# Kernel tuning notes

Measured on AMD Instinct MI355X. Metric: run time of the kernel, lower is better.

The kernel has to match this reference:

```python
import jax, jax.numpy as jnp
import numpy as np

B, N, D, E, R, K = 4, 2048, 1024, 8, 256, 2


def setup_inputs() -> dict:
    key = jax.random.key(0)
    ks = jax.random.split(key, 5)
    scale = 0.02
    return {
        "x": jax.random.normal(ks[0], (B, N, D), dtype=jnp.float32),
        "gate_w": jax.random.normal(ks[1], (D, E), dtype=jnp.float32) * scale,
        "Wu": jax.random.normal(ks[2], (E, D, R), dtype=jnp.float32) * scale,
        "Wv": jax.random.normal(ks[3], (E, D, R), dtype=jnp.float32) * scale,
        "Wo": jax.random.normal(ks[4], (E, R, D), dtype=jnp.float32) * scale,
    }


def reference(x, gate_w, Wu, Wv, Wo):
    # Router: top-k over expert logits, softmax over the selected k logits.
    logits = jnp.einsum("bnd,de->bne", x, gate_w)          # [B,N,E]
    topv, topi = jax.lax.top_k(logits, K)                    # [B,N,K]
    w = jax.nn.softmax(topv, axis=-1)                        # [B,N,K]

    # Dense all-expert SwiGLU (matches reference semantics: every expert
    # computed for every token, then gathered by top-k index).
    u = jnp.einsum("bnd,edr->bner", x, Wu)                  # [B,N,E,R]
    v = jnp.einsum("bnd,edr->bner", x, Wv)                  # [B,N,E,R]
    s = jax.nn.silu(u) * v                                   # [B,N,E,R]
    Y = jnp.einsum("bner,erd->bned", s, Wo)                 # [B,N,E,D]

    # Gather the k selected experts per token and combine with gate weights.
    y_sel = jnp.take_along_axis(Y, topi[..., None], axis=2)  # [B,N,K,D]
    out = jnp.einsum("bnkd,bnk->bnd", y_sel, w)             # [B,N,D]
    return out
```

## Files before the change

### kernel.cpp

```cpp
#include <hip/hip_runtime.h>
#include <math.h>

#define BN 8192
#define DIM 1024
#define NE 8
#define RR 256

using bf16x8 = __attribute__((ext_vector_type(8))) short;
using f32x4  = __attribute__((ext_vector_type(4))) float;

#define GLD16(g, l) __builtin_amdgcn_global_load_lds(                      \
    (const __attribute__((address_space(1))) void*)(g),                    \
    (__attribute__((address_space(3))) void*)(l), 16, 0, 0)

__device__ inline unsigned short f2bf(float f) {
    unsigned int u = __float_as_uint(f);
    u = (u + 0x7fffu + ((u >> 16) & 1u)) >> 16;
    return (unsigned short)u;
}

__global__ __launch_bounds__(256) void k_gwt(const float* __restrict__ gw,
                                             float* __restrict__ gwT) {
    int i = blockIdx.x * 256 + threadIdx.x;
    float v = gw[i];
    int d = i >> 3, e = i & 7;
    gwT[e * DIM + d] = v;
}

__global__ __launch_bounds__(256) void k_router3(const float* __restrict__ x,
                                                 const float* __restrict__ gwT,
                                                 int* __restrict__ topi,
                                                 float* __restrict__ topw,
                                                 unsigned short* __restrict__ xb) {
    int wid  = (blockIdx.x * blockDim.x + threadIdx.x) >> 6;
    int lane = threadIdx.x & 63;
    const float* xp = x + (size_t)wid * DIM + lane * 4;
    unsigned short* xbp = xb + (size_t)wid * DIM + lane * 4;
    float4 acc[NE];
#pragma unroll
    for (int e = 0; e < NE; ++e) acc[e] = float4{0.f, 0.f, 0.f, 0.f};
#pragma unroll
    for (int k = 0; k < 4; ++k) {
        float4 xv = *(const float4*)(xp + k * 256);
        ushort4 us = { f2bf(xv.x), f2bf(xv.y), f2bf(xv.z), f2bf(xv.w) };
        *(ushort4*)(xbp + k * 256) = us;
#pragma unroll
        for (int e = 0; e < NE; ++e) {
            float4 gv = *(const float4*)(gwT + e * DIM + k * 256 + lane * 4);
            acc[e].x += xv.x * gv.x; acc[e].y += xv.y * gv.y;
            acc[e].z += xv.z * gv.z; acc[e].w += xv.w * gv.w;
        }
    }
    float lg[NE];
#pragma unroll
    for (int e = 0; e < NE; ++e)
        lg[e] = (acc[e].x + acc[e].y) + (acc[e].z + acc[e].w);
#pragma unroll
    for (int off = 32; off; off >>= 1) {
#pragma unroll
        for (int e = 0; e < NE; ++e) lg[e] += __shfl_xor(lg[e], off, 64);
    }
    if (lane == 0) {
        float best = lg[0]; int bi = 0;
#pragma unroll
        for (int e = 1; e < NE; ++e) if (lg[e] > best) { best = lg[e]; bi = e; }
        float sec = -3.4e38f; int si = 0;
#pragma unroll
        for (int e = 0; e < NE; ++e) if (e != bi && lg[e] > sec) { sec = lg[e]; si = e; }
        float p  = __expf(sec - best);
        float w0 = 1.f / (1.f + p);
        float w1 = p * w0;
        topi[wid * 2 + 0] = bi;  topw[wid * 2 + 0] = w0;
        topi[wid * 2 + 1] = si;  topw[wid * 2 + 1] = w1;
    }
}

__global__ __launch_bounds__(1024) void k_count_scan(const int* __restrict__ topi,
                                                     int* __restrict__ counts,
                                                     int* __restrict__ offsets,
                                                     int* __restrict__ fill,
                                                     int* __restrict__ tileOff) {
    __shared__ int sh[1024 * NE];
    int tid = threadIdx.x;
    int c[NE];
#pragma unroll
    for (int j = 0; j < NE; ++j) c[j] = 0;
    const int4* tp = (const int4*)topi;
    for (int i = tid; i < BN * 2 / 4; i += 1024) {
        int4 v = tp[i];
#pragma unroll
        for (int j = 0; j < NE; ++j)
            c[j] += (v.x == j) + (v.y == j) + (v.z == j) + (v.w == j);
    }
#pragma unroll
    for (int j = 0; j < NE; ++j) sh[tid * NE + j] = c[j];
    __syncthreads();
    for (int s = 512; s > 0; s >>= 1) {
        if (tid < s) {
#pragma unroll
            for (int j = 0; j < NE; ++j) sh[tid * NE + j] += sh[(tid + s) * NE + j];
        }
        __syncthreads();
    }
    if (tid == 0) {
        int acc = 0, tacc = 0;
        for (int j = 0; j < NE; ++j) {
            int cj = sh[j];
            counts[j]  = cj;
            offsets[j] = acc;   acc  += cj;
            tileOff[j] = tacc;  tacc += (cj + 127) >> 7;
        }
        tileOff[NE] = tacc;
    }
    if (tid < NE) fill[tid] = 0;
}

__global__ __launch_bounds__(256) void k_fill2(const int* __restrict__ topi,
                                               const float* __restrict__ topw,
                                               const int* __restrict__ offsets,
                                               int* __restrict__ fill,
                                               int* __restrict__ btok,
                                               float* __restrict__ bw,
                                               int* __restrict__ slotOf) {
    int tid = threadIdx.x;
    int i = blockIdx.x * 256 + tid;
    int w = tid >> 6, lane = tid & 63;
    int e = topi[i];
    float wt = topw[i];

    __shared__ int waveCnt[4][NE];
    __shared__ int wavePre[4][NE];
    __shared__ int baseSh[NE];

    int myrank = 0;
    unsigned long long lt = (1ull << lane) - 1ull;
#pragma unroll
    for (int j = 0; j < NE; ++j) {
        unsigned long long m = __ballot(e == j);
        if (e == j) myrank = __popcll(m & lt);
        if (lane == 0) waveCnt[w][j] = __popcll(m);
    }
    __syncthreads();
    if (tid < NE) {
        int j = tid, acc = 0;
#pragma unroll
        for (int ww = 0; ww < 4; ++ww) { wavePre[ww][j] = acc; acc += waveCnt[ww][j]; }
        baseSh[j] = atomicAdd(&fill[j], acc);
    }
    __syncthreads();
    int slot = offsets[e] + baseSh[e] + wavePre[w][e] + myrank;
    btok[slot] = i >> 1;
    bw[slot]   = wt;
    slotOf[i]  = slot;
}

__global__ __launch_bounds__(256) void k_cvt3(const float* __restrict__ Wu,
                                              const float* __restrict__ Wv,
                                              const float* __restrict__ Wo,
                                              unsigned short* __restrict__ Wub,
                                              unsigned short* __restrict__ Wvb,
                                              unsigned short* __restrict__ Wob) {
    int z = blockIdx.y;
    int which = z >> 3, e = z & 7;
    int tile = blockIdx.x;
    const float* in; unsigned short* out;
    int M, N, n0, m0;
    if (which < 2) {
        M = DIM; N = RR;
        n0 = (tile & 7) * 32;  m0 = (tile >> 3) * 32;
        in = which ? Wv : Wu;  out = which ? Wvb : Wub;
    } else {
        M = RR; N = DIM;
        n0 = (tile & 31) * 32; m0 = (tile >> 5) * 32;
        in = Wo; out = Wob;
    }
    __shared__ float t[32][33];
    int tx = threadIdx.x & 31, ty = threadIdx.x >> 5;
    const float* inE = in + (size_t)e * M * N;
    unsigned short* outE = out + (size_t)e * M * N;
#pragma unroll
    for (int i = ty; i < 32; i += 8)
        t[i][tx] = inE[(size_t)(m0 + i) * N + n0 + tx];
    __syncthreads();
#pragma unroll
    for (int i = ty; i < 32; i += 8)
        outE[(size_t)(n0 + i) * M + m0 + tx] = f2bf(t[tx][i]);
}

__global__ __launch_bounds__(256, 2) void k_uv(
        const unsigned short* __restrict__ xb,
        const unsigned short* __restrict__ Wub,
        const unsigned short* __restrict__ Wvb,
        const int* __restrict__ counts,
        const int* __restrict__ offsets,
        const int* __restrict__ tileOff,
        const int* __restrict__ btok,
        const float* __restrict__ bw,
        unsigned short* __restrict__ Sbuf) {
    int bid = blockIdx.x;
    int lt  = (bid & 7) * 68 + (bid >> 3);
    int rt  = lt & 3;
    int mt_lin = lt >> 2;
    if (mt_lin >= tileOff[NE]) return;
    int e = 0;
#pragma unroll
    for (int j = 1; j < NE; ++j) if (mt_lin >= tileOff[j]) e = j;
    int t0 = (mt_lin - tileOff[e]) * 128;
    int ne = counts[e];
    int nt = min(128, ne - t0);
    int start = offsets[e] + t0;

    int tid = threadIdx.x;
    int w = tid >> 6, lane = tid & 63;
    int m16 = lane & 15, quad = lane >> 4;
    int wm = w & 1, wn = w >> 1;

    __shared__ unsigned short As[128][64];
    __shared__ unsigned short Bs[128][64];
    __shared__ int   tokL[128];
    __shared__ float gwL[128];

    if (tid < 128) {
        tokL[tid] = (tid < nt) ? btok[start + tid] : btok[start];
        gwL[tid]  = (tid < nt) ? bw[start + tid] : 0.f;
    }
    __syncthreads();

    int rc0 = rt * 64;
    const unsigned short* WuE = Wub + (size_t)e * RR * DIM;
    const unsigned short* WvE = Wvb + (size_t)e * RR * DIM;

    const unsigned short* aS[4];
    const unsigned short* bS[4];
    int dstOff[4];
#pragma unroll
    for (int i = 0; i < 4; ++i) {
        int chunk = w * 4 + i;
        int row = chunk * 8 + (lane >> 3);
        int js  = (lane & 7) ^ (row & 7);
        aS[i] = xb + (size_t)tokL[row] * DIM + js * 8;
        bS[i] = ((row < 64) ? (WuE + (size_t)(rc0 + row) * DIM)
                            : (WvE + (size_t)(rc0 + row - 64) * DIM)) + js * 8;
        dstOff[i] = chunk * 1024;
    }
    auto* asb = (__attribute__((address_space(3))) char*)&As[0][0];
    auto* bsb = (__attribute__((address_space(3))) char*)&Bs[0][0];
    const char* Ab = (const char*)&As[0][0];
    const char* Bb = (const char*)&Bs[0][0];

    f32x4 accU[4][2], accV[4][2];
    f32x4 zz = {0.f, 0.f, 0.f, 0.f};
#pragma unroll
    for (int mt = 0; mt < 4; ++mt)
#pragma unroll
        for (int nl = 0; nl < 2; ++nl) { accU[mt][nl] = zz; accV[mt][nl] = zz; }

    for (int kt = 0; kt < 16; ++kt) {
        if (kt) __syncthreads();
#pragma unroll
        for (int i = 0; i < 4; ++i) {
            GLD16(aS[i] + kt * 64, asb + dstOff[i]);
            GLD16(bS[i] + kt * 64, bsb + dstOff[i]);
        }
        __syncthreads();
#pragma unroll
        for (int ks = 0; ks < 2; ++ks) {
            bf16x8 a[4], bu[2], bv[2];
#pragma unroll
            for (int mt = 0; mt < 4; ++mt) {
                int r = wm * 64 + mt * 16 + m16;
                int u = (ks * 4 + quad) ^ (r & 7);
                a[mt] = *(const bf16x8*)(Ab + r * 128 + u * 16);
            }
#pragma unroll
            for (int nl = 0; nl < 2; ++nl) {
                int r = wn * 32 + nl * 16 + m16;
                int u = (ks * 4 + quad) ^ (r & 7);
                bu[nl] = *(const bf16x8*)(Bb + r * 128 + u * 16);
                bv[nl] = *(const bf16x8*)(Bb + (r + 64) * 128 + u * 16);
            }
#pragma unroll
            for (int nl = 0; nl < 2; ++nl)
#pragma unroll
                for (int mt = 0; mt < 4; ++mt) {
                    accU[mt][nl] = __builtin_amdgcn_mfma_f32_16x16x32_bf16(a[mt], bu[nl], accU[mt][nl], 0, 0, 0);
                    accV[mt][nl] = __builtin_amdgcn_mfma_f32_16x16x32_bf16(a[mt], bv[nl], accV[mt][nl], 0, 0, 0);
                }
        }
    }

#pragma unroll
    for (int mt = 0; mt < 4; ++mt)
#pragma unroll
        for (int nl = 0; nl < 2; ++nl)
#pragma unroll
            for (int reg = 0; reg < 4; ++reg) {
                int trow = wm * 64 + mt * 16 + quad * 4 + reg;
                int rcol = rc0 + wn * 32 + nl * 16 + m16;
                float u = accU[mt][nl][reg], v = accV[mt][nl][reg];
                float s = (u / (1.f + __expf(-u))) * v * gwL[trow];
                if (trow < nt)
                    Sbuf[(size_t)(start + trow) * RR + rcol] = f2bf(s);
            }
}

__global__ __launch_bounds__(256, 2) void k_down(
        const unsigned short* __restrict__ Sbuf,
        const unsigned short* __restrict__ Wob,
        const int* __restrict__ counts,
        const int* __restrict__ offsets,
        const int* __restrict__ tileOff,
        const int* __restrict__ btok,
        float* __restrict__ ybuf,
        float* __restrict__ out) {
    int bid = blockIdx.x;
    int lt  = (bid & 7) * 136 + (bid >> 3);
    int nd = lt & 7;
    int mt_lin = lt >> 3;
    if (mt_lin >= tileOff[NE]) return;
    int e = 0;
#pragma unroll
    for (int j = 1; j < NE; ++j) if (mt_lin >= tileOff[j]) e = j;
    int t0 = (mt_lin - tileOff[e]) * 128;
    int ne = counts[e];
    int nt = min(128, ne - t0);
    int start = offsets[e] + t0;

    int tid = threadIdx.x;
    int w = tid >> 6, lane = tid & 63;
    int m16 = lane & 15, quad = lane >> 4;
    int wm = w & 1, wn = w >> 1;

    __shared__ unsigned short As[128][64];
    __shared__ unsigned short Bs[128][64];
    __shared__ int tokL[128];

    if (tid < 128)
        tokL[tid] = (tid < nt) ? btok[start + tid] : btok[start];
    __syncthreads();

    const unsigned short* WoE = Wob + (size_t)e * DIM * RR;

    const unsigned short* aS[4];
    const unsigned short* bS[4];
    int dstOff[4];
#pragma unroll
    for (int i = 0; i < 4; ++i) {
        int chunk = w * 4 + i;
        int row = chunk * 8 + (lane >> 3);
        int js  = (lane & 7) ^ (row & 7);
        aS[i] = Sbuf + (size_t)(start + row) * RR + js * 8;
        bS[i] = WoE + (size_t)(nd * 128 + row) * RR + js * 8;
        dstOff[i] = chunk * 1024;
    }
    auto* asb = (__attribute__((address_space(3))) char*)&As[0][0];
    auto* bsb = (__attribute__((address_space(3))) char*)&Bs[0][0];
    const char* Ab = (const char*)&As[0][0];
    const char* Bb = (const char*)&Bs[0][0];

    f32x4 acc[4][4];
    f32x4 zz = {0.f, 0.f, 0.f, 0.f};
#pragma unroll
    for (int mt = 0; mt < 4; ++mt)
#pragma unroll
        for (int nl = 0; nl < 4; ++nl) acc[mt][nl] = zz;

    for (int kt = 0; kt < 4; ++kt) {
        if (kt) __syncthreads();
#pragma unroll
        for (int i = 0; i < 4; ++i) {
            GLD16(aS[i] + kt * 64, asb + dstOff[i]);
            GLD16(bS[i] + kt * 64, bsb + dstOff[i]);
        }
        __syncthreads();
#pragma unroll
        for (int ks = 0; ks < 2; ++ks) {
            bf16x8 a[4], b[4];
#pragma unroll
            for (int mt = 0; mt < 4; ++mt) {
                int r = wm * 64 + mt * 16 + m16;
                int u = (ks * 4 + quad) ^ (r & 7);
                a[mt] = *(const bf16x8*)(Ab + r * 128 + u * 16);
            }
#pragma unroll
            for (int nl = 0; nl < 4; ++nl) {
                int r = wn * 64 + nl * 16 + m16;
                int u = (ks * 4 + quad) ^ (r & 7);
                b[nl] = *(const bf16x8*)(Bb + r * 128 + u * 16);
            }
#pragma unroll
            for (int nl = 0; nl < 4; ++nl)
#pragma unroll
                for (int mt = 0; mt < 4; ++mt)
                    acc[mt][nl] = __builtin_amdgcn_mfma_f32_16x16x32_bf16(a[mt], b[nl], acc[mt][nl], 0, 0, 0);
        }
    }

    if (ybuf) {
#pragma unroll
        for (int mt = 0; mt < 4; ++mt)
#pragma unroll
            for (int nl = 0; nl < 4; ++nl)
#pragma unroll
                for (int reg = 0; reg < 4; ++reg) {
                    int srow = wm * 64 + mt * 16 + quad * 4 + reg;
                    int d    = nd * 128 + wn * 64 + nl * 16 + m16;
                    if (srow < nt)
                        ybuf[(size_t)(start + srow) * DIM + d] = acc[mt][nl][reg];
                }
    } else {
#pragma unroll
        for (int mt = 0; mt < 4; ++mt)
#pragma unroll
            for (int nl = 0; nl < 4; ++nl)
#pragma unroll
                for (int reg = 0; reg < 4; ++reg) {
                    int srow = wm * 64 + mt * 16 + quad * 4 + reg;
                    int d    = nd * 128 + wn * 64 + nl * 16 + m16;
                    if (srow < nt)
                        atomicAdd(&out[(size_t)tokL[srow] * DIM + d], acc[mt][nl][reg]);
                }
    }
}

__global__ __launch_bounds__(256) void k_combine(const float* __restrict__ ybuf,
                                                 const int* __restrict__ slotOf,
                                                 float* __restrict__ out) {
    int t   = blockIdx.x;
    int seg = threadIdx.x;
    int s0 = slotOf[t * 2 + 0];
    int s1 = slotOf[t * 2 + 1];
    float4 a = *(const float4*)(ybuf + (size_t)s0 * DIM + seg * 4);
    float4 b = *(const float4*)(ybuf + (size_t)s1 * DIM + seg * 4);
    float4 r = { a.x + b.x, a.y + b.y, a.z + b.z, a.w + b.w };
    *(float4*)(out + (size_t)t * DIM + seg * 4) = r;
}

extern "C" void kernel_launch(void* const* d_in, const int* in_sizes, int n_in,
                              void* d_out, int out_size, void* d_ws, size_t ws_size,
                              hipStream_t stream) {
    const float* x  = (const float*)d_in[0];
    const float* gw = (const float*)d_in[1];
    const float* Wu = (const float*)d_in[2];
    const float* Wv = (const float*)d_in[3];
    const float* Wo = (const float*)d_in[4];
    float* out = (float*)d_out;

    int*   wsi     = (int*)d_ws;
    int*   counts  = wsi + 0;
    int*   offsets = wsi + 8;
    int*   fill    = wsi + 16;
    int*   tileOff = wsi + 24;
    int*   topi    = wsi + 48;
    float* topw    = (float*)(wsi + 48 + 16384);
    int*   btok    = wsi + 48 + 32768;
    float* bw      = (float*)(wsi + 48 + 49152);
    int*   slotOf  = wsi + 48 + 65536;
    float* gwT     = (float*)((char*)d_ws + 327872);

    const size_t off_xb  = 393216;
    const size_t off_wub = off_xb  + (size_t)BN * DIM * 2;
    const size_t off_wvb = off_wub + (size_t)NE * RR * DIM * 2;
    const size_t off_wob = off_wvb + (size_t)NE * RR * DIM * 2;
    const size_t off_sb  = off_wob + (size_t)NE * DIM * RR * 2;
    const size_t off_yb  = off_sb  + (size_t)(BN * 2 + 128) * RR * 2;
    const size_t need_yb = off_yb  + (size_t)BN * 2 * DIM * 4;

    unsigned short* xb   = (unsigned short*)((char*)d_ws + off_xb);
    unsigned short* Wub  = (unsigned short*)((char*)d_ws + off_wub);
    unsigned short* Wvb  = (unsigned short*)((char*)d_ws + off_wvb);
    unsigned short* Wob  = (unsigned short*)((char*)d_ws + off_wob);
    unsigned short* Sbuf = (unsigned short*)((char*)d_ws + off_sb);
    bool use_ybuf = (ws_size >= need_yb);
    float* ybuf = use_ybuf ? (float*)((char*)d_ws + off_yb) : nullptr;

    k_gwt<<<dim3(DIM * NE / 256), 256, 0, stream>>>(gw, gwT);
    k_router3<<<dim3(BN / 4), 256, 0, stream>>>(x, gwT, topi, topw, xb);
    k_count_scan<<<1, 1024, 0, stream>>>(topi, counts, offsets, fill, tileOff);
    k_fill2<<<dim3(BN * 2 / 256), 256, 0, stream>>>(topi, topw, offsets, fill,
                                                    btok, bw, slotOf);
    k_cvt3<<<dim3(256, 24), 256, 0, stream>>>(Wu, Wv, Wo, Wub, Wvb, Wob);

    if (!use_ybuf)
        hipMemsetAsync(d_out, 0, (size_t)BN * DIM * sizeof(float), stream);

    k_uv<<<dim3(544), 256, 0, stream>>>(xb, Wub, Wvb, counts, offsets, tileOff,
                                        btok, bw, Sbuf);
    k_down<<<dim3(1088), 256, 0, stream>>>(Sbuf, Wob, counts, offsets, tileOff,
                                           btok, ybuf, out);
    if (use_ybuf)
        k_combine<<<dim3(BN), 256, 0, stream>>>(ybuf, slotOf, out);
}
```

Before: 195.7 us.

## Double-buffer LDS tiles in up and down projection GEMM kernels

Both grouped expert GEMM kernels now keep two LDS buffers for the A and B tiles. Each iteration issues the async global-to-LDS loads for the next k-tile before running MFMAs on the current one, with one barrier per iteration instead of two. The goal is to hide global load latency behind compute. It doubles LDS use per block (64KB), which may reduce occupancy. It also relies on the barrier waiting for the async LDS loads to finish.

```diff
diff --git a/kernel.cpp b/kernel.cpp
--- a/kernel.cpp
+++ b/kernel.cpp
@@ -215,8 +215,8 @@
     int m16 = lane & 15, quad = lane >> 4;
     int wm = w & 1, wn = w >> 1;
 
-    __shared__ unsigned short As[128][64];
-    __shared__ unsigned short Bs[128][64];
+    __shared__ unsigned short As[2][128][64];
+    __shared__ unsigned short Bs[2][128][64];
     __shared__ int   tokL[128];
     __shared__ float gwL[128];
 
@@ -243,10 +243,18 @@
                             : (WvE + (size_t)(rc0 + row - 64) * DIM)) + js * 8;
         dstOff[i] = chunk * 1024;
     }
-    auto* asb = (__attribute__((address_space(3))) char*)&As[0][0];
-    auto* bsb = (__attribute__((address_space(3))) char*)&Bs[0][0];
-    const char* Ab = (const char*)&As[0][0];
-    const char* Bb = (const char*)&Bs[0][0];
+    auto* asb = (__attribute__((address_space(3))) char*)&As[0][0][0];
+    auto* bsb = (__attribute__((address_space(3))) char*)&Bs[0][0][0];
+    const char* Ab = (const char*)&As[0][0][0];
+    const char* Bb = (const char*)&Bs[0][0][0];
+
+    auto stage = [&](int buf, int kt) {
+#pragma unroll
+        for (int i = 0; i < 4; ++i) {
+            GLD16(aS[i] + kt * 64, asb + buf * 16384 + dstOff[i]);
+            GLD16(bS[i] + kt * 64, bsb + buf * 16384 + dstOff[i]);
+        }
+    };
 
     f32x4 accU[4][2], accV[4][2];
     f32x4 zz = {0.f, 0.f, 0.f, 0.f};
@@ -255,14 +263,11 @@
 #pragma unroll
         for (int nl = 0; nl < 2; ++nl) { accU[mt][nl] = zz; accV[mt][nl] = zz; }
 
+    stage(0, 0);
+    __syncthreads();
     for (int kt = 0; kt < 16; ++kt) {
-        if (kt) __syncthreads();
-#pragma unroll
-        for (int i = 0; i < 4; ++i) {
-            GLD16(aS[i] + kt * 64, asb + dstOff[i]);
-            GLD16(bS[i] + kt * 64, bsb + dstOff[i]);
-        }
-        __syncthreads();
+        const int cur = kt & 1;
+        if (kt < 15) stage(cur ^ 1, kt + 1);
 #pragma unroll
         for (int ks = 0; ks < 2; ++ks) {
             bf16x8 a[4], bu[2], bv[2];
@@ -270,14 +275,14 @@
             for (int mt = 0; mt < 4; ++mt) {
                 int r = wm * 64 + mt * 16 + m16;
                 int u = (ks * 4 + quad) ^ (r & 7);
-                a[mt] = *(const bf16x8*)(Ab + r * 128 + u * 16);
+                a[mt] = *(const bf16x8*)(Ab + cur * 16384 + r * 128 + u * 16);
             }
 #pragma unroll
             for (int nl = 0; nl < 2; ++nl) {
                 int r = wn * 32 + nl * 16 + m16;
                 int u = (ks * 4 + quad) ^ (r & 7);
-                bu[nl] = *(const bf16x8*)(Bb + r * 128 + u * 16);
-                bv[nl] = *(const bf16x8*)(Bb + (r + 64) * 128 + u * 16);
+                bu[nl] = *(const bf16x8*)(Bb + cur * 16384 + r * 128 + u * 16);
+                bv[nl] = *(const bf16x8*)(Bb + cur * 16384 + (r + 64) * 128 + u * 16);
             }
 #pragma unroll
             for (int nl = 0; nl < 2; ++nl)
@@ -287,6 +292,7 @@
                     accV[mt][nl] = __builtin_amdgcn_mfma_f32_16x16x32_bf16(a[mt], bv[nl], accV[mt][nl], 0, 0, 0);
                 }
         }
+        __syncthreads();
     }
 
 #pragma unroll
@@ -331,8 +337,8 @@
     int m16 = lane & 15, quad = lane >> 4;
     int wm = w & 1, wn = w >> 1;
 
-    __shared__ unsigned short As[128][64];
-    __shared__ unsigned short Bs[128][64];
+    __shared__ unsigned short As[2][128][64];
+    __shared__ unsigned short Bs[2][128][64];
     __shared__ int tokL[128];
 
     if (tid < 128)
@@ -353,10 +359,18 @@
         bS[i] = WoE + (size_t)(nd * 128 + row) * RR + js * 8;
         dstOff[i] = chunk * 1024;
     }
-    auto* asb = (__attribute__((address_space(3))) char*)&As[0][0];
-    auto* bsb = (__attribute__((address_space(3))) char*)&Bs[0][0];
-    const char* Ab = (const char*)&As[0][0];
-    const char* Bb = (const char*)&Bs[0][0];
+    auto* asb = (__attribute__((address_space(3))) char*)&As[0][0][0];
+    auto* bsb = (__attribute__((address_space(3))) char*)&Bs[0][0][0];
+    const char* Ab = (const char*)&As[0][0][0];
+    const char* Bb = (const char*)&Bs[0][0][0];
+
+    auto stage = [&](int buf, int kt) {
+#pragma unroll
+        for (int i = 0; i < 4; ++i) {
+            GLD16(aS[i] + kt * 64, asb + buf * 16384 + dstOff[i]);
+            GLD16(bS[i] + kt * 64, bsb + buf * 16384 + dstOff[i]);
+        }
+    };
 
     f32x4 acc[4][4];
     f32x4 zz = {0.f, 0.f, 0.f, 0.f};
@@ -365,14 +379,11 @@
 #pragma unroll
         for (int nl = 0; nl < 4; ++nl) acc[mt][nl] = zz;
 
+    stage(0, 0);
+    __syncthreads();
     for (int kt = 0; kt < 4; ++kt) {
-        if (kt) __syncthreads();
-#pragma unroll
-        for (int i = 0; i < 4; ++i) {
-            GLD16(aS[i] + kt * 64, asb + dstOff[i]);
-            GLD16(bS[i] + kt * 64, bsb + dstOff[i]);
-        }
-        __syncthreads();
+        const int cur = kt & 1;
+        if (kt < 3) stage(cur ^ 1, kt + 1);
 #pragma unroll
         for (int ks = 0; ks < 2; ++ks) {
             bf16x8 a[4], b[4];
@@ -380,13 +391,13 @@
             for (int mt = 0; mt < 4; ++mt) {
                 int r = wm * 64 + mt * 16 + m16;
                 int u = (ks * 4 + quad) ^ (r & 7);
-                a[mt] = *(const bf16x8*)(Ab + r * 128 + u * 16);
+                a[mt] = *(const bf16x8*)(Ab + cur * 16384 + r * 128 + u * 16);
             }
 #pragma unroll
             for (int nl = 0; nl < 4; ++nl) {
                 int r = wn * 64 + nl * 16 + m16;
                 int u = (ks * 4 + quad) ^ (r & 7);
-                b[nl] = *(const bf16x8*)(Bb + r * 128 + u * 16);
+                b[nl] = *(const bf16x8*)(Bb + cur * 16384 + r * 128 + u * 16);
             }
 #pragma unroll
             for (int nl = 0; nl < 4; ++nl)
@@ -394,6 +405,7 @@
                 for (int mt = 0; mt < 4; ++mt)
                     acc[mt][nl] = __builtin_amdgcn_mfma_f32_16x16x32_bf16(a[mt], b[nl], acc[mt][nl], 0, 0, 0);
         }
+        __syncthreads();
     }
 
     if (ybuf) {
```

After: 209.2 us. +6.9%, slower.

## Fuse expert counting into router and drop gate-weight transpose kernel

Applied to the files above, without the earlier changes.

The router now reads gate_w in its native [D,E] layout, so the separate transpose kernel goes away. Per-expert counts are accumulated inside the router with shared-memory atomics followed by one global atomic per block. This replaces the single-block 1024-thread count/scan kernel with a tiny scan kernel and a memset that zeros counts and fill. The aim is fewer launches and less serial single-block work, at the cost of global atomics and a different gate-weight access pattern.

```diff
diff --git a/kernel.cpp b/kernel.cpp
--- a/kernel.cpp
+++ b/kernel.cpp
@@ -19,47 +19,44 @@
     return (unsigned short)u;
 }
 
-__global__ __launch_bounds__(256) void k_gwt(const float* __restrict__ gw,
-                                             float* __restrict__ gwT) {
-    int i = blockIdx.x * 256 + threadIdx.x;
-    float v = gw[i];
-    int d = i >> 3, e = i & 7;
-    gwT[e * DIM + d] = v;
-}
-
 __global__ __launch_bounds__(256) void k_router3(const float* __restrict__ x,
-                                                 const float* __restrict__ gwT,
+                                                 const float* __restrict__ gw,
                                                  int* __restrict__ topi,
                                                  float* __restrict__ topw,
-                                                 unsigned short* __restrict__ xb) {
+                                                 unsigned short* __restrict__ xb,
+                                                 int* __restrict__ counts) {
     int wid  = (blockIdx.x * blockDim.x + threadIdx.x) >> 6;
     int lane = threadIdx.x & 63;
     const float* xp = x + (size_t)wid * DIM + lane * 4;
     unsigned short* xbp = xb + (size_t)wid * DIM + lane * 4;
-    float4 acc[NE];
-#pragma unroll
-    for (int e = 0; e < NE; ++e) acc[e] = float4{0.f, 0.f, 0.f, 0.f};
+    float lg[NE];
+#pragma unroll
+    for (int e = 0; e < NE; ++e) lg[e] = 0.f;
 #pragma unroll
     for (int k = 0; k < 4; ++k) {
         float4 xv = *(const float4*)(xp + k * 256);
         ushort4 us = { f2bf(xv.x), f2bf(xv.y), f2bf(xv.z), f2bf(xv.w) };
         *(ushort4*)(xbp + k * 256) = us;
-#pragma unroll
-        for (int e = 0; e < NE; ++e) {
-            float4 gv = *(const float4*)(gwT + e * DIM + k * 256 + lane * 4);
-            acc[e].x += xv.x * gv.x; acc[e].y += xv.y * gv.y;
-            acc[e].z += xv.z * gv.z; acc[e].w += xv.w * gv.w;
-        }
-    }
-    float lg[NE];
-#pragma unroll
-    for (int e = 0; e < NE; ++e)
-        lg[e] = (acc[e].x + acc[e].y) + (acc[e].z + acc[e].w);
+        const float* gp = gw + (size_t)(k * 256 + lane * 4) * NE;
+#pragma unroll
+        for (int j = 0; j < 4; ++j) {
+            float xj = (j == 0) ? xv.x : (j == 1) ? xv.y : (j == 2) ? xv.z : xv.w;
+            float4 g0 = *(const float4*)(gp + j * NE);
+            float4 g1 = *(const float4*)(gp + j * NE + 4);
+            lg[0] += xj * g0.x; lg[1] += xj * g0.y;
+            lg[2] += xj * g0.z; lg[3] += xj * g0.w;
+            lg[4] += xj * g1.x; lg[5] += xj * g1.y;
+            lg[6] += xj * g1.z; lg[7] += xj * g1.w;
+        }
+    }
 #pragma unroll
     for (int off = 32; off; off >>= 1) {
 #pragma unroll
         for (int e = 0; e < NE; ++e) lg[e] += __shfl_xor(lg[e], off, 64);
     }
+    __shared__ int bc[NE];
+    if (threadIdx.x < NE) bc[threadIdx.x] = 0;
+    __syncthreads();
     if (lane == 0) {
         float best = lg[0]; int bi = 0;
 #pragma unroll
@@ -72,47 +69,28 @@
         float w1 = p * w0;
         topi[wid * 2 + 0] = bi;  topw[wid * 2 + 0] = w0;
         topi[wid * 2 + 1] = si;  topw[wid * 2 + 1] = w1;
-    }
-}
-
-__global__ __launch_bounds__(1024) void k_count_scan(const int* __restrict__ topi,
-                                                     int* __restrict__ counts,
-                                                     int* __restrict__ offsets,
-                                                     int* __restrict__ fill,
-                                                     int* __restrict__ tileOff) {
-    __shared__ int sh[1024 * NE];
-    int tid = threadIdx.x;
-    int c[NE];
-#pragma unroll
-    for (int j = 0; j < NE; ++j) c[j] = 0;
-    const int4* tp = (const int4*)topi;
-    for (int i = tid; i < BN * 2 / 4; i += 1024) {
-        int4 v = tp[i];
-#pragma unroll
-        for (int j = 0; j < NE; ++j)
-            c[j] += (v.x == j) + (v.y == j) + (v.z == j) + (v.w == j);
-    }
-#pragma unroll
-    for (int j = 0; j < NE; ++j) sh[tid * NE + j] = c[j];
-    __syncthreads();
-    for (int s = 512; s > 0; s >>= 1) {
-        if (tid < s) {
-#pragma unroll
-            for (int j = 0; j < NE; ++j) sh[tid * NE + j] += sh[(tid + s) * NE + j];
-        }
-        __syncthreads();
-    }
-    if (tid == 0) {
+        atomicAdd(&bc[bi], 1);
+        atomicAdd(&bc[si], 1);
+    }
+    __syncthreads();
+    if (threadIdx.x < NE) {
+        int c = bc[threadIdx.x];
+        if (c) atomicAdd(&counts[threadIdx.x], c);
+    }
+}
+
+__global__ __launch_bounds__(64) void k_scan(const int* __restrict__ counts,
+                                             int* __restrict__ offsets,
+                                             int* __restrict__ tileOff) {
+    if (threadIdx.x == 0) {
         int acc = 0, tacc = 0;
         for (int j = 0; j < NE; ++j) {
-            int cj = sh[j];
-            counts[j]  = cj;
+            int cj = counts[j];
             offsets[j] = acc;   acc  += cj;
             tileOff[j] = tacc;  tacc += (cj + 127) >> 7;
         }
         tileOff[NE] = tacc;
     }
-    if (tid < NE) fill[tid] = 0;
 }
 
 __global__ __launch_bounds__(256) void k_fill2(const int* __restrict__ topi,
@@ -456,7 +434,6 @@
     int*   btok    = wsi + 48 + 32768;
     float* bw      = (float*)(wsi + 48 + 49152);
     int*   slotOf  = wsi + 48 + 65536;
-    float* gwT     = (float*)((char*)d_ws + 327872);
 
     const size_t off_xb  = 393216;
     const size_t off_wub = off_xb  + (size_t)BN * DIM * 2;
@@ -474,9 +451,10 @@
     bool use_ybuf = (ws_size >= need_yb);
     float* ybuf = use_ybuf ? (float*)((char*)d_ws + off_yb) : nullptr;
 
-    k_gwt<<<dim3(DIM * NE / 256), 256, 0, stream>>>(gw, gwT);
-    k_router3<<<dim3(BN / 4), 256, 0, stream>>>(x, gwT, topi, topw, xb);
-    k_count_scan<<<1, 1024, 0, stream>>>(topi, counts, offsets, fill, tileOff);
+    hipMemsetAsync(wsi, 0, 192, stream);
+
+    k_router3<<<dim3(BN / 4), 256, 0, stream>>>(x, gw, topi, topw, xb, counts);
+    k_scan<<<1, 64, 0, stream>>>(counts, offsets, tileOff);
     k_fill2<<<dim3(BN * 2 / 256), 256, 0, stream>>>(topi, topw, offsets, fill,
                                                     btok, bw, slotOf);
     k_cvt3<<<dim3(256, 24), 256, 0, stream>>>(Wu, Wv, Wo, Wub, Wvb, Wob);
```

After: 206.6 us. 5.5% more time.
